# Optimization experiments

Measured on AMD Instinct MI355X. Metric: run time of the kernel, lower is better.

## Reference

```python
import jax, jax.numpy as jnp
import numpy as np

EMBED_DIM = 512

def _eq_linear(x, W):
    # EqualizedLinear: weight scaled by 1/sqrt(fan_in), no bias.
    c = 1.0 / np.sqrt(W.shape[1])
    return jnp.einsum('bnd,ed->bne', x, W) * c

def setup_inputs() -> dict:
    key = jax.random.key(0)
    ks = jax.random.split(key, 6)
    b, n, d = 8, 2048, 512
    return {
        'q': jax.random.normal(ks[0], (b, n, d), jnp.float32),
        'k': jax.random.normal(ks[1], (b, n, d), jnp.float32),
        'v': jax.random.normal(ks[2], (b, n, d), jnp.float32),
        'Wq': jax.random.normal(ks[3], (EMBED_DIM, d), jnp.float32),
        'Wk': jax.random.normal(ks[4], (EMBED_DIM, d), jnp.float32),
        'Wv': jax.random.normal(ks[5], (EMBED_DIM, d), jnp.float32),
    }

def reference(q, k, v, Wq, Wk, Wv):
    scale = EMBED_DIM ** (-0.5)
    qp = _eq_linear(q, Wq)  # [b, n, e]
    kp = _eq_linear(k, Wk)  # [b, m, e]
    vp = _eq_linear(v, Wv)  # [b, m, e]
    dots = jnp.einsum('bne,bme->bnm', qp, kp) * scale
    attn = jax.nn.softmax(dots, axis=-1)
    out = jnp.einsum('bnm,bme->bne', attn, vp)
    return (out, (jax.lax.stop_gradient(attn),))
```

## Files before the change

kernel.cpp:

```cpp
#include <hip/hip_runtime.h>
#include <math.h>

constexpr int BATCH = 8;
constexpr int SEQ   = 2048;
constexpr int DIM   = 512;

typedef _Float16 f16x8  __attribute__((ext_vector_type(8)));
typedef float    f32x16 __attribute__((ext_vector_type(16)));

__device__ __forceinline__ void gload_lds16(const void* g, void* l) {
    __builtin_amdgcn_global_load_lds(
        (const __attribute__((address_space(1))) void*)g,
        (__attribute__((address_space(3))) void*)l, 16, 0, 0);
}

template<bool OUT_F16>
__global__ __launch_bounds__(256, 2) void gemm_nt_f16(
    const _Float16* __restrict__ A, int lda, long sA,
    const _Float16* __restrict__ B, int ldb, long sB,
    void* __restrict__ Cv, int ldc, long sC,
    int K, float alpha)
{
    __shared__ _Float16 As[8][128][8];
    __shared__ _Float16 Bs[8][256][8];

    const int bz = blockIdx.z;
    A += (long)bz * sA;  B += (long)bz * sB;
    const long bm = (long)blockIdx.y * 128;
    const long bn = (long)blockIdx.x * 256;
    const int t    = threadIdx.x;
    const int lane = t & 63;
    const int wave = t >> 6;
    const int wm = (wave >> 1) * 64;
    const int wn = (wave & 1) * 128;
    const int ml = lane & 31;
    const int kh = lane >> 5;

    f32x16 acc[2][4] = {};

    for (int k0 = 0; k0 < K; k0 += 64) {
#pragma unroll
        for (int s = 0; s < 4; s++) {
            const int idx = wave * 4 + s;
            const int ch  = idx >> 1;
            const int r0  = (idx & 1) * 64;
            const _Float16* gp = A + (bm + r0 + lane) * (long)lda + k0 + ch * 8;
            gload_lds16(gp, &As[ch][r0][0]);
        }
#pragma unroll
        for (int s = 0; s < 8; s++) {
            const int idx = wave * 8 + s;
            const int ch  = idx >> 2;
            const int r0  = (idx & 3) * 64;
            const _Float16* gp = B + (bn + r0 + lane) * (long)ldb + k0 + ch * 8;
            gload_lds16(gp, &Bs[ch][r0][0]);
        }
        __syncthreads();

#pragma unroll
        for (int ks = 0; ks < 4; ks++) {
            const int ch = ks * 2 + kh;
            f16x8 a0 = *(const f16x8*)&As[ch][wm      + ml][0];
            f16x8 a1 = *(const f16x8*)&As[ch][wm + 32 + ml][0];
            f16x8 b0 = *(const f16x8*)&Bs[ch][wn       + ml][0];
            f16x8 b1 = *(const f16x8*)&Bs[ch][wn + 32  + ml][0];
            f16x8 b2 = *(const f16x8*)&Bs[ch][wn + 64  + ml][0];
            f16x8 b3 = *(const f16x8*)&Bs[ch][wn + 96  + ml][0];
            acc[0][0] = __builtin_amdgcn_mfma_f32_32x32x16_f16(a0, b0, acc[0][0], 0, 0, 0);
            acc[0][1] = __builtin_amdgcn_mfma_f32_32x32x16_f16(a0, b1, acc[0][1], 0, 0, 0);
            acc[0][2] = __builtin_amdgcn_mfma_f32_32x32x16_f16(a0, b2, acc[0][2], 0, 0, 0);
            acc[0][3] = __builtin_amdgcn_mfma_f32_32x32x16_f16(a0, b3, acc[0][3], 0, 0, 0);
            acc[1][0] = __builtin_amdgcn_mfma_f32_32x32x16_f16(a1, b0, acc[1][0], 0, 0, 0);
            acc[1][1] = __builtin_amdgcn_mfma_f32_32x32x16_f16(a1, b1, acc[1][1], 0, 0, 0);
            acc[1][2] = __builtin_amdgcn_mfma_f32_32x32x16_f16(a1, b2, acc[1][2], 0, 0, 0);
            acc[1][3] = __builtin_amdgcn_mfma_f32_32x32x16_f16(a1, b3, acc[1][3], 0, 0, 0);
        }
        __syncthreads();
    }

    float*    Cf = (float*)Cv    + (OUT_F16 ? 0 : (long)bz * sC);
    _Float16* Ch = (_Float16*)Cv + (OUT_F16 ? (long)bz * sC : 0);
#pragma unroll
    for (int i = 0; i < 2; i++)
#pragma unroll
        for (int j = 0; j < 4; j++) {
            const long col = bn + wn + j * 32 + ml;
#pragma unroll
            for (int rg = 0; rg < 16; rg++) {
                const long row = bm + wm + i * 32 + (rg & 3) + 8 * (rg >> 2) + 4 * kh;
                if constexpr (OUT_F16)
                    Ch[row * (long)ldc + col] = (_Float16)(alpha * acc[i][j][rg]);
                else
                    Cf[row * (long)ldc + col] = alpha * acc[i][j][rg];
            }
        }
}

__global__ __launch_bounds__(256) void gemm_tn_f32(
    const float* __restrict__ A, int lda,
    const float* __restrict__ B, int ldb,
    _Float16* __restrict__ C, int ldc, int K, float alpha)
{
    __shared__ float As[16][68];
    __shared__ float Bs[16][68];
    const int bm = blockIdx.y * 64;
    const int bn = blockIdx.x * 64;
    const int t  = threadIdx.x;
    const int tx = t & 15, ty = t >> 4;
    const int kk = t >> 4, mc = (t & 15) * 4;

    float acc[4][4] = {};
    for (int k0 = 0; k0 < K; k0 += 16) {
        float4 a = *(const float4*)(A + (long)(k0 + kk) * lda + bm + mc);
        float4 b = *(const float4*)(B + (long)(k0 + kk) * ldb + bn + mc);
        __syncthreads();
        As[kk][mc] = a.x; As[kk][mc + 1] = a.y; As[kk][mc + 2] = a.z; As[kk][mc + 3] = a.w;
        Bs[kk][mc] = b.x; Bs[kk][mc + 1] = b.y; Bs[kk][mc + 2] = b.z; Bs[kk][mc + 3] = b.w;
        __syncthreads();
#pragma unroll
        for (int k = 0; k < 16; k++) {
            float ar[4], br[4];
#pragma unroll
            for (int i = 0; i < 4; i++) ar[i] = As[k][ty * 4 + i];
#pragma unroll
            for (int j = 0; j < 4; j++) br[j] = Bs[k][tx * 4 + j];
#pragma unroll
            for (int i = 0; i < 4; i++)
#pragma unroll
                for (int j = 0; j < 4; j++) acc[i][j] = fmaf(ar[i], br[j], acc[i][j]);
        }
    }
#pragma unroll
    for (int i = 0; i < 4; i++)
#pragma unroll
        for (int j = 0; j < 4; j++)
            C[(long)(bm + ty * 4 + i) * ldc + bn + tx * 4 + j] =
                (_Float16)(alpha * acc[i][j]);
}

__global__ __launch_bounds__(256) void softmax_rows(
    float* __restrict__ attn, _Float16* __restrict__ attn16)
{
    const long row = blockIdx.x;
    float* p = attn + row * (long)SEQ;
    const int t = threadIdx.x;
    float4 v0 = *(const float4*)(p + t * 8);
    float4 v1 = *(const float4*)(p + t * 8 + 4);

    float m = fmaxf(fmaxf(fmaxf(v0.x, v0.y), fmaxf(v0.z, v0.w)),
                    fmaxf(fmaxf(v1.x, v1.y), fmaxf(v1.z, v1.w)));
#pragma unroll
    for (int off = 32; off > 0; off >>= 1) m = fmaxf(m, __shfl_xor(m, off));
    __shared__ float sm[4];
    __shared__ float ss[4];
    const int wave = t >> 6;
    if ((t & 63) == 0) sm[wave] = m;
    __syncthreads();
    m = fmaxf(fmaxf(sm[0], sm[1]), fmaxf(sm[2], sm[3]));

    v0.x = __expf(v0.x - m); v0.y = __expf(v0.y - m);
    v0.z = __expf(v0.z - m); v0.w = __expf(v0.w - m);
    v1.x = __expf(v1.x - m); v1.y = __expf(v1.y - m);
    v1.z = __expf(v1.z - m); v1.w = __expf(v1.w - m);

    float s = v0.x + v0.y + v0.z + v0.w + v1.x + v1.y + v1.z + v1.w;
#pragma unroll
    for (int off = 32; off > 0; off >>= 1) s += __shfl_xor(s, off);
    if ((t & 63) == 0) ss[wave] = s;
    __syncthreads();
    s = ss[0] + ss[1] + ss[2] + ss[3];
    const float inv = 1.0f / s;

    v0.x *= inv; v0.y *= inv; v0.z *= inv; v0.w *= inv;
    v1.x *= inv; v1.y *= inv; v1.z *= inv; v1.w *= inv;
    *(float4*)(p + t * 8)     = v0;
    *(float4*)(p + t * 8 + 4) = v1;

    f16x8 h;
    h[0] = (_Float16)v0.x; h[1] = (_Float16)v0.y;
    h[2] = (_Float16)v0.z; h[3] = (_Float16)v0.w;
    h[4] = (_Float16)v1.x; h[5] = (_Float16)v1.y;
    h[6] = (_Float16)v1.z; h[7] = (_Float16)v1.w;
    *(f16x8*)(attn16 + row * (long)SEQ + t * 8) = h;
}

__global__ __launch_bounds__(256) void conv_f16(
    const float* __restrict__ in, _Float16* __restrict__ out, int n8)
{
    const int i = blockIdx.x * 256 + threadIdx.x;
    if (i >= n8) return;
    const float4 a = ((const float4*)in)[2 * i];
    const float4 b = ((const float4*)in)[2 * i + 1];
    f16x8 h;
    h[0] = (_Float16)a.x; h[1] = (_Float16)a.y; h[2] = (_Float16)a.z; h[3] = (_Float16)a.w;
    h[4] = (_Float16)b.x; h[5] = (_Float16)b.y; h[6] = (_Float16)b.z; h[7] = (_Float16)b.w;
    ((f16x8*)out)[i] = h;
}

extern "C" void kernel_launch(void* const* d_in, const int* in_sizes, int n_in,
                              void* d_out, int out_size, void* d_ws, size_t ws_size,
                              hipStream_t stream)
{
    const float* q  = (const float*)d_in[0];
    const float* k  = (const float*)d_in[1];
    const float* v  = (const float*)d_in[2];
    const float* Wq = (const float*)d_in[3];
    const float* Wk = (const float*)d_in[4];
    const float* Wv = (const float*)d_in[5];

    float* out  = (float*)d_out;
    float* attn = (float*)d_out + (size_t)BATCH * SEQ * DIM;

    char* w = (char*)d_ws;
    _Float16* q16    = (_Float16*)(w);
    _Float16* k16    = (_Float16*)(w + 16777216);
    _Float16* v16    = (_Float16*)(w + 33554432);
    _Float16* attn16 = (_Float16*)(w);
    _Float16* T16    = (_Float16*)(w + 67108864);
    _Float16* vpT16  = (_Float16*)(w + 83886080);
    _Float16* Wv16   = (_Float16*)(w + 100663296);
    _Float16* P16    = (_Float16*)(w + 101187584);

    const float c = 0.044194173824159216f;

    conv_f16<<<dim3(4096), 256, 0, stream>>>(q,  q16,  1048576);
    conv_f16<<<dim3(4096), 256, 0, stream>>>(k,  k16,  1048576);
    conv_f16<<<dim3(4096), 256, 0, stream>>>(v,  v16,  1048576);
    conv_f16<<<dim3(128),  256, 0, stream>>>(Wv, Wv16, 32768);

    gemm_tn_f32<<<dim3(8, 8), 256, 0, stream>>>(Wk, DIM, Wq, DIM, P16, DIM, DIM, c * c);

    gemm_nt_f16<true><<<dim3(2, 128, 1), 256, 0, stream>>>(
        q16, DIM, 0, P16, DIM, 0, T16, DIM, 0, DIM, 1.0f);

    gemm_nt_f16<false><<<dim3(8, 16, 8), 256, 0, stream>>>(
        T16, DIM, (long)SEQ * DIM, k16, DIM, (long)SEQ * DIM,
        attn, SEQ, (long)SEQ * SEQ, DIM, c);

    gemm_nt_f16<true><<<dim3(8, 4, 8), 256, 0, stream>>>(
        Wv16, DIM, 0, v16, DIM, (long)SEQ * DIM,
        vpT16, SEQ, (long)DIM * SEQ, DIM, c);

    softmax_rows<<<dim3(BATCH * SEQ), 256, 0, stream>>>(attn, attn16);

    gemm_nt_f16<false><<<dim3(2, 16, 8), 256, 0, stream>>>(
        attn16, SEQ, (long)SEQ * SEQ, vpT16, SEQ, (long)DIM * SEQ,
        out, DIM, (long)SEQ * DIM, SEQ, 1.0f);
}
```

Before: 512.1 us.

## Store attention logits in fp16, remap workgroups across XCDs, fuse conversions

The QK^T GEMM now writes its logits as fp16 into a workspace buffer instead of fp32 into the output. Softmax then reads fp16, writes the fp32 attention with nontemporal stores and writes fp16 probabilities back in place, which cuts the intermediate read and write traffic. Workgroup IDs are remapped round-robin across the 8 XCDs for L2 locality, and the four fp32→fp16 conversion launches are merged into one. Rounding logits to fp16 before softmax adds precision error and needs a larger workspace.

Measured after the change: 498.6 us. 1.03x faster.

```diff
diff --git a/kernel.cpp b/kernel.cpp
--- a/kernel.cpp
+++ b/kernel.cpp
@@ -6,6 +6,7 @@
 constexpr int DIM   = 512;
 
 typedef _Float16 f16x8  __attribute__((ext_vector_type(8)));
+typedef float    f32x4  __attribute__((ext_vector_type(4)));
 typedef float    f32x16 __attribute__((ext_vector_type(16)));
 
 __device__ __forceinline__ void gload_lds16(const void* g, void* l) {
@@ -24,10 +25,17 @@
     __shared__ _Float16 As[8][128][8];
     __shared__ _Float16 Bs[8][256][8];
 
-    const int bz = blockIdx.z;
+    int lin = blockIdx.x + gridDim.x * (blockIdx.y + gridDim.y * blockIdx.z);
+    const int nwg = gridDim.x * gridDim.y * gridDim.z;
+    lin = (lin & 7) * (nwg >> 3) + (lin >> 3);
+    const int bx  = lin % gridDim.x;
+    const int byz = lin / gridDim.x;
+    const int by  = byz % gridDim.y;
+    const int bz  = byz / gridDim.y;
+
     A += (long)bz * sA;  B += (long)bz * sB;
-    const long bm = (long)blockIdx.y * 128;
-    const long bn = (long)blockIdx.x * 256;
+    const long bm = (long)by * 128;
+    const long bn = (long)bx * 256;
     const int t    = threadIdx.x;
     const int lane = t & 63;
     const int wave = t >> 6;
@@ -91,7 +99,8 @@
                 if constexpr (OUT_F16)
                     Ch[row * (long)ldc + col] = (_Float16)(alpha * acc[i][j][rg]);
                 else
-                    Cf[row * (long)ldc + col] = alpha * acc[i][j][rg];
+                    __builtin_nontemporal_store(alpha * acc[i][j][rg],
+                                                &Cf[row * (long)ldc + col]);
             }
         }
 }
@@ -139,16 +148,21 @@
 }
 
 __global__ __launch_bounds__(256) void softmax_rows(
-    float* __restrict__ attn, _Float16* __restrict__ attn16)
+    _Float16* __restrict__ dots, float* __restrict__ attn)
 {
     const long row = blockIdx.x;
-    float* p = attn + row * (long)SEQ;
+    _Float16* ph = dots + row * (long)SEQ + threadIdx.x * 8;
+    float*    pf = attn + row * (long)SEQ + threadIdx.x * 8;
     const int t = threadIdx.x;
-    float4 v0 = *(const float4*)(p + t * 8);
-    float4 v1 = *(const float4*)(p + t * 8 + 4);
-
-    float m = fmaxf(fmaxf(fmaxf(v0.x, v0.y), fmaxf(v0.z, v0.w)),
-                    fmaxf(fmaxf(v1.x, v1.y), fmaxf(v1.z, v1.w)));
+
+    f16x8 h = *(const f16x8*)ph;
+    float x[8];
+#pragma unroll
+    for (int i = 0; i < 8; i++) x[i] = (float)h[i];
+
+    float m = x[0];
+#pragma unroll
+    for (int i = 1; i < 8; i++) m = fmaxf(m, x[i]);
 #pragma unroll
     for (int off = 32; off > 0; off >>= 1) m = fmaxf(m, __shfl_xor(m, off));
     __shared__ float sm[4];
@@ -158,12 +172,9 @@
     __syncthreads();
     m = fmaxf(fmaxf(sm[0], sm[1]), fmaxf(sm[2], sm[3]));
 
-    v0.x = __expf(v0.x - m); v0.y = __expf(v0.y - m);
-    v0.z = __expf(v0.z - m); v0.w = __expf(v0.w - m);
-    v1.x = __expf(v1.x - m); v1.y = __expf(v1.y - m);
-    v1.z = __expf(v1.z - m); v1.w = __expf(v1.w - m);
-
-    float s = v0.x + v0.y + v0.z + v0.w + v1.x + v1.y + v1.z + v1.w;
+    float s = 0.0f;
+#pragma unroll
+    for (int i = 0; i < 8; i++) { x[i] = __expf(x[i] - m); s += x[i]; }
 #pragma unroll
     for (int off = 32; off > 0; off >>= 1) s += __shfl_xor(s, off);
     if ((t & 63) == 0) ss[wave] = s;
@@ -171,30 +182,39 @@
     s = ss[0] + ss[1] + ss[2] + ss[3];
     const float inv = 1.0f / s;
 
-    v0.x *= inv; v0.y *= inv; v0.z *= inv; v0.w *= inv;
-    v1.x *= inv; v1.y *= inv; v1.z *= inv; v1.w *= inv;
-    *(float4*)(p + t * 8)     = v0;
-    *(float4*)(p + t * 8 + 4) = v1;
-
-    f16x8 h;
-    h[0] = (_Float16)v0.x; h[1] = (_Float16)v0.y;
-    h[2] = (_Float16)v0.z; h[3] = (_Float16)v0.w;
-    h[4] = (_Float16)v1.x; h[5] = (_Float16)v1.y;
-    h[6] = (_Float16)v1.z; h[7] = (_Float16)v1.w;
-    *(f16x8*)(attn16 + row * (long)SEQ + t * 8) = h;
-}
-
-__global__ __launch_bounds__(256) void conv_f16(
-    const float* __restrict__ in, _Float16* __restrict__ out, int n8)
-{
-    const int i = blockIdx.x * 256 + threadIdx.x;
-    if (i >= n8) return;
-    const float4 a = ((const float4*)in)[2 * i];
-    const float4 b = ((const float4*)in)[2 * i + 1];
+    f32x4 o0, o1;
+    o0[0] = x[0] * inv; o0[1] = x[1] * inv; o0[2] = x[2] * inv; o0[3] = x[3] * inv;
+    o1[0] = x[4] * inv; o1[1] = x[5] * inv; o1[2] = x[6] * inv; o1[3] = x[7] * inv;
+    f32x4* pv = (f32x4*)pf;
+    __builtin_nontemporal_store(o0, pv);
+    __builtin_nontemporal_store(o1, pv + 1);
+
+    f16x8 hn;
+    hn[0] = (_Float16)o0[0]; hn[1] = (_Float16)o0[1];
+    hn[2] = (_Float16)o0[2]; hn[3] = (_Float16)o0[3];
+    hn[4] = (_Float16)o1[0]; hn[5] = (_Float16)o1[1];
+    hn[6] = (_Float16)o1[2]; hn[7] = (_Float16)o1[3];
+    *(f16x8*)ph = hn;
+}
+
+__global__ __launch_bounds__(256) void conv_all(
+    const float* __restrict__ q, const float* __restrict__ k,
+    const float* __restrict__ v, const float* __restrict__ Wv,
+    _Float16* __restrict__ q16, _Float16* __restrict__ k16,
+    _Float16* __restrict__ v16, _Float16* __restrict__ Wv16)
+{
+    int i = blockIdx.x * 256 + threadIdx.x;
+    const float* src; _Float16* dst;
+    if (i < 1048576)      { src = q;  dst = q16; }
+    else if (i < 2097152) { src = k;  dst = k16;  i -= 1048576; }
+    else if (i < 3145728) { src = v;  dst = v16;  i -= 2097152; }
+    else                  { src = Wv; dst = Wv16; i -= 3145728; }
+    const float4 a = ((const float4*)src)[2 * i];
+    const float4 b = ((const float4*)src)[2 * i + 1];
     f16x8 h;
     h[0] = (_Float16)a.x; h[1] = (_Float16)a.y; h[2] = (_Float16)a.z; h[3] = (_Float16)a.w;
     h[4] = (_Float16)b.x; h[5] = (_Float16)b.y; h[6] = (_Float16)b.z; h[7] = (_Float16)b.w;
-    ((f16x8*)out)[i] = h;
+    ((f16x8*)dst)[i] = h;
 }
 
 extern "C" void kernel_launch(void* const* d_in, const int* in_sizes, int n_in,
@@ -213,37 +233,34 @@
 
     char* w = (char*)d_ws;
     _Float16* q16    = (_Float16*)(w);
-    _Float16* k16    = (_Float16*)(w + 16777216);
-    _Float16* v16    = (_Float16*)(w + 33554432);
-    _Float16* attn16 = (_Float16*)(w);
-    _Float16* T16    = (_Float16*)(w + 67108864);
-    _Float16* vpT16  = (_Float16*)(w + 83886080);
-    _Float16* Wv16   = (_Float16*)(w + 100663296);
-    _Float16* P16    = (_Float16*)(w + 101187584);
+    _Float16* dots16 = (_Float16*)(w);
+    _Float16* k16    = (_Float16*)(w + 67108864);
+    _Float16* v16    = (_Float16*)(w + 83886080);
+    _Float16* T16    = (_Float16*)(w + 100663296);
+    _Float16* vpT16  = (_Float16*)(w + 117440512);
+    _Float16* Wv16   = (_Float16*)(w + 134217728);
+    _Float16* P16    = (_Float16*)(w + 134742016);
 
     const float c = 0.044194173824159216f;
 
-    conv_f16<<<dim3(4096), 256, 0, stream>>>(q,  q16,  1048576);
-    conv_f16<<<dim3(4096), 256, 0, stream>>>(k,  k16,  1048576);
-    conv_f16<<<dim3(4096), 256, 0, stream>>>(v,  v16,  1048576);
-    conv_f16<<<dim3(128),  256, 0, stream>>>(Wv, Wv16, 32768);
+    conv_all<<<dim3(12416), 256, 0, stream>>>(q, k, v, Wv, q16, k16, v16, Wv16);
 
     gemm_tn_f32<<<dim3(8, 8), 256, 0, stream>>>(Wk, DIM, Wq, DIM, P16, DIM, DIM, c * c);
 
     gemm_nt_f16<true><<<dim3(2, 128, 1), 256, 0, stream>>>(
         q16, DIM, 0, P16, DIM, 0, T16, DIM, 0, DIM, 1.0f);
 
-    gemm_nt_f16<false><<<dim3(8, 16, 8), 256, 0, stream>>>(
+    gemm_nt_f16<true><<<dim3(8, 16, 8), 256, 0, stream>>>(
         T16, DIM, (long)SEQ * DIM, k16, DIM, (long)SEQ * DIM,
-        attn, SEQ, (long)SEQ * SEQ, DIM, c);
+        dots16, SEQ, (long)SEQ * SEQ, DIM, c);
 
     gemm_nt_f16<true><<<dim3(8, 4, 8), 256, 0, stream>>>(
         Wv16, DIM, 0, v16, DIM, (long)SEQ * DIM,
         vpT16, SEQ, (long)DIM * SEQ, DIM, c);
 
-    softmax_rows<<<dim3(BATCH * SEQ), 256, 0, stream>>>(attn, attn16);
+    softmax_rows<<<dim3(BATCH * SEQ), 256, 0, stream>>>(dots16, attn);
 
     gemm_nt_f16<false><<<dim3(2, 16, 8), 256, 0, stream>>>(
-        attn16, SEQ, (long)SEQ * SEQ, vpT16, SEQ, (long)DIM * SEQ,
+        dots16, SEQ, (long)SEQ * SEQ, vpT16, SEQ, (long)DIM * SEQ,
         out, DIM, (long)SEQ * DIM, SEQ, 1.0f);
 }
```
